# Kernel optimization log

Hardware: AMD Instinct MI355X
Metric: run time of the kernel (lower is better)

## Reference

```python
import jax, jax.numpy as jnp
import numpy as np

N_NODES = 50000
N_EDGES = 800000
H = 128
FF = 4 * H
SCALE = 30.0
EPS = 1e-5


def _layer_norm(x, g, b):
    mu = jnp.mean(x, axis=-1, keepdims=True)
    var = jnp.mean((x - mu) ** 2, axis=-1, keepdims=True)
    return (x - mu) * jax.lax.rsqrt(var + EPS) * g + b


def _linear(x, W, b):
    return x @ W.T + b


def setup_inputs() -> dict:
    key = jax.random.key(0)
    ks = jax.random.split(key, 16)
    s = lambda fan_in: 1.0 / np.sqrt(fan_in)
    inp = {
        "h_V": jax.random.normal(ks[0], (N_NODES, H), jnp.float32),
        "h_E": jax.random.normal(ks[1], (N_EDGES, H), jnp.float32),
        "src_idx": jax.random.randint(ks[2], (N_EDGES,), 0, N_NODES),
        "batch_id": jnp.zeros((N_NODES,), jnp.int32),
        "dst_idx": jax.random.randint(ks[3], (N_EDGES,), 0, N_NODES),
        "W1": jax.random.uniform(ks[4], (H, 3 * H), jnp.float32, -s(3 * H), s(3 * H)),
        "b1": jnp.zeros((H,), jnp.float32),
        "W2": jax.random.uniform(ks[5], (H, H), jnp.float32, -s(H), s(H)),
        "b2": jnp.zeros((H,), jnp.float32),
        "W3": jax.random.uniform(ks[6], (H, H), jnp.float32, -s(H), s(H)),
        "b3": jnp.zeros((H,), jnp.float32),
        "ln1_g": jnp.ones((H,), jnp.float32),
        "ln1_b": jnp.zeros((H,), jnp.float32),
        "ln2_g": jnp.ones((H,), jnp.float32),
        "ln2_b": jnp.zeros((H,), jnp.float32),
        "W_in": jax.random.uniform(ks[7], (FF, H), jnp.float32, -s(H), s(H)),
        "b_in": jnp.zeros((FF,), jnp.float32),
        "W_out": jax.random.uniform(ks[8], (H, FF), jnp.float32, -s(FF), s(FF)),
        "b_out": jnp.zeros((H,), jnp.float32),
    }
    return inp


def reference(h_V, h_E, src_idx, batch_id, dst_idx,
              W1, b1, W2, b2, W3, b3,
              ln1_g, ln1_b, ln2_g, ln2_b,
              W_in, b_in, W_out, b_out):
    # gather + concat: [E, 3H]
    h_EV = jnp.concatenate([h_V[src_idx], h_E, h_V[dst_idx]], axis=-1)
    # 3-layer edge MLP (exact GELU, matching torch default)
    h = jax.nn.gelu(_linear(h_EV, W1, b1), approximate=False)
    h = jax.nn.gelu(_linear(h, W2, b2), approximate=False)
    h_message = _linear(h, W3, b3)
    # scatter_mean by src_idx over N_NODES segments
    seg_sum = jax.ops.segment_sum(h_message, src_idx, num_segments=N_NODES)
    cnt = jax.ops.segment_sum(jnp.ones((h_message.shape[0],), h_message.dtype),
                              src_idx, num_segments=N_NODES)
    dh = seg_sum / jnp.maximum(cnt, 1.0)[:, None] / SCALE
    # residual + norm (dropout = identity in eval)
    h_V = _layer_norm(h_V + dh, ln1_g, ln1_b)
    # FFN
    dh = _linear(jax.nn.gelu(_linear(h_V, W_in, b_in), approximate=False), W_out, b_out)
    h_V = _layer_norm(h_V + dh, ln2_g, ln2_b)
    return h_V
```

## Files before the change

### kernel.cpp

```cpp
#include <hip/hip_runtime.h>

#define NE 800000
#define NN 50000
#define HD 128
#define FFD 512

typedef __bf16 bf16;
typedef bf16 bf16x8 __attribute__((ext_vector_type(8)));
typedef float f32x4 __attribute__((ext_vector_type(4)));

__device__ __forceinline__ float gelu_f(float x) {
    return 0.5f * x * (1.0f + erff(x * 0.70710678118654752f));
}

__device__ __forceinline__ bf16x8 cvt8(f32x4 a, f32x4 b) {
    bf16x8 t;
    t[0] = (bf16)a[0]; t[1] = (bf16)a[1]; t[2] = (bf16)a[2]; t[3] = (bf16)a[3];
    t[4] = (bf16)b[0]; t[5] = (bf16)b[1]; t[6] = (bf16)b[2]; t[7] = (bf16)b[3];
    return t;
}

__global__ void cvt_weights(const float* __restrict__ W1, const float* __restrict__ W2,
                            const float* __restrict__ W3, const float* __restrict__ Win,
                            const float* __restrict__ Wout, bf16* __restrict__ o) {
    int i = blockIdx.x * 256 + threadIdx.x;
    if (i < 49152)        o[i] = (bf16)W1[i];
    else if (i < 65536)   o[i] = (bf16)W2[i - 49152];
    else if (i < 81920)   o[i] = (bf16)W3[i - 65536];
    else if (i < 147456)  o[i] = (bf16)Win[i - 81920];
    else if (i < 212992)  o[i] = (bf16)Wout[i - 147456];
}

__global__ void hist_kernel(const int* __restrict__ src, int* __restrict__ cnt) {
    int i = blockIdx.x * 256 + threadIdx.x;
    if (i < NE) atomicAdd(cnt + src[i], 1);
}

__global__ __launch_bounds__(1024) void scan_kernel(const int* __restrict__ cnt,
                                                    int* __restrict__ head) {
    __shared__ int wsum[16];
    __shared__ int carry;
    const int tid = threadIdx.x, lane = tid & 63, w = tid >> 6;
    if (tid == 0) carry = 0;
    __syncthreads();
    for (int base = 0; base < NN; base += 1024) {
        int i = base + tid;
        int v = (i < NN) ? cnt[i] : 0;
        int x = v;
#pragma unroll
        for (int m = 1; m < 64; m <<= 1) {
            int y = __shfl_up(x, m, 64);
            if (lane >= m) x += y;
        }
        if (lane == 63) wsum[w] = x;
        __syncthreads();
        if (w == 0) {
            int s = (lane < 16) ? wsum[lane] : 0;
#pragma unroll
            for (int m = 1; m < 16; m <<= 1) {
                int y = __shfl_up(s, m, 64);
                if (lane >= m) s += y;
            }
            if (lane < 16) wsum[lane] = s;
        }
        __syncthreads();
        int excl = carry + (w > 0 ? wsum[w - 1] : 0) + x - v;
        if (i < NN) head[i] = excl;
        int total = wsum[15];
        __syncthreads();
        if (tid == 0) carry += total;
        __syncthreads();
    }
}

__global__ void scatter_perm(const int* __restrict__ src, int* __restrict__ head,
                             int* __restrict__ perm) {
    int i = blockIdx.x * 256 + threadIdx.x;
    if (i < NE) {
        int pos = atomicAdd(head + src[i], 1);
        perm[pos] = i;
    }
}

__global__ __launch_bounds__(256, 2) void edge_mlp(
    const float* __restrict__ hV, const float* __restrict__ hE,
    const int* __restrict__ src, const int* __restrict__ dst,
    const int* __restrict__ perm,
    const bf16* __restrict__ W1b, const bf16* __restrict__ W2b, const bf16* __restrict__ W3b,
    const float* __restrict__ b1, const float* __restrict__ b2, const float* __restrict__ b3,
    float* __restrict__ segsum)
{
    __shared__ __align__(16) char smem[128 * 132 * 4];
    bf16  (*lx)[136] = (bf16 (*)[136])smem;
    float (*lz)[132] = (float (*)[132])smem;
    __shared__ int ssrc[128];

    const int tid  = threadIdx.x;
    const int wave = tid >> 6, lane = tid & 63;
    const int wr = wave >> 1, wc = wave & 1;
    const int quad = lane >> 4, l16 = lane & 15;
    const int row0 = blockIdx.x * 128;

    if (tid < 128) ssrc[tid] = src[perm[row0 + tid]];

    int arow[4], asrc[4], adst[4];
#pragma unroll
    for (int rt = 0; rt < 4; ++rt) {
        int e = perm[row0 + wr * 64 + rt * 16 + l16];
        arow[rt] = e; asrc[rt] = src[e]; adst[rt] = dst[e];
    }

    f32x4 acc[4][4];
#pragma unroll
    for (int i = 0; i < 4; ++i)
#pragma unroll
        for (int j = 0; j < 4; ++j) acc[i][j] = (f32x4){0.f, 0.f, 0.f, 0.f};

#pragma unroll
    for (int ks = 0; ks < 12; ++ks) {
        const int k = ks * 32 + quad * 8;
        bf16x8 a[4];
#pragma unroll
        for (int rt = 0; rt < 4; ++rt) {
            const float* p;
            if (ks < 4)      p = hV + (size_t)asrc[rt] * HD + k;
            else if (ks < 8) p = hE + (size_t)arow[rt] * HD + (k - 128);
            else             p = hV + (size_t)adst[rt] * HD + (k - 256);
            f32x4 f0 = *(const f32x4*)p;
            f32x4 f1 = *(const f32x4*)(p + 4);
            a[rt] = cvt8(f0, f1);
        }
        bf16x8 b[4];
#pragma unroll
        for (int ct = 0; ct < 4; ++ct) {
            int col = wc * 64 + ct * 16 + l16;
            b[ct] = *(const bf16x8*)(W1b + (size_t)col * 384 + ks * 32 + quad * 8);
        }
#pragma unroll
        for (int rt = 0; rt < 4; ++rt)
#pragma unroll
            for (int ct = 0; ct < 4; ++ct)
                acc[rt][ct] = __builtin_amdgcn_mfma_f32_16x16x32_bf16(a[rt], b[ct], acc[rt][ct], 0, 0, 0);
    }

#pragma unroll
    for (int ct = 0; ct < 4; ++ct) {
        int col = wc * 64 + ct * 16 + l16;
        float bias = b1[col];
#pragma unroll
        for (int rt = 0; rt < 4; ++rt)
#pragma unroll
            for (int r = 0; r < 4; ++r)
                lx[wr * 64 + rt * 16 + quad * 4 + r][col] = (bf16)gelu_f(acc[rt][ct][r] + bias);
    }
    __syncthreads();

#pragma unroll
    for (int i = 0; i < 4; ++i)
#pragma unroll
        for (int j = 0; j < 4; ++j) acc[i][j] = (f32x4){0.f, 0.f, 0.f, 0.f};
#pragma unroll
    for (int ks = 0; ks < 4; ++ks) {
        bf16x8 a[4], b[4];
#pragma unroll
        for (int rt = 0; rt < 4; ++rt)
            a[rt] = *(const bf16x8*)&lx[wr * 64 + rt * 16 + l16][ks * 32 + quad * 8];
#pragma unroll
        for (int ct = 0; ct < 4; ++ct)
            b[ct] = *(const bf16x8*)(W2b + (size_t)(wc * 64 + ct * 16 + l16) * HD + ks * 32 + quad * 8);
#pragma unroll
        for (int rt = 0; rt < 4; ++rt)
#pragma unroll
            for (int ct = 0; ct < 4; ++ct)
                acc[rt][ct] = __builtin_amdgcn_mfma_f32_16x16x32_bf16(a[rt], b[ct], acc[rt][ct], 0, 0, 0);
    }
    __syncthreads();

#pragma unroll
    for (int ct = 0; ct < 4; ++ct) {
        int col = wc * 64 + ct * 16 + l16;
        float bias = b2[col];
#pragma unroll
        for (int rt = 0; rt < 4; ++rt)
#pragma unroll
            for (int r = 0; r < 4; ++r)
                lx[wr * 64 + rt * 16 + quad * 4 + r][col] = (bf16)gelu_f(acc[rt][ct][r] + bias);
    }
    __syncthreads();

#pragma unroll
    for (int i = 0; i < 4; ++i)
#pragma unroll
        for (int j = 0; j < 4; ++j) acc[i][j] = (f32x4){0.f, 0.f, 0.f, 0.f};
#pragma unroll
    for (int ks = 0; ks < 4; ++ks) {
        bf16x8 a[4], b[4];
#pragma unroll
        for (int rt = 0; rt < 4; ++rt)
            a[rt] = *(const bf16x8*)&lx[wr * 64 + rt * 16 + l16][ks * 32 + quad * 8];
#pragma unroll
        for (int ct = 0; ct < 4; ++ct)
            b[ct] = *(const bf16x8*)(W3b + (size_t)(wc * 64 + ct * 16 + l16) * HD + ks * 32 + quad * 8);
#pragma unroll
        for (int rt = 0; rt < 4; ++rt)
#pragma unroll
            for (int ct = 0; ct < 4; ++ct)
                acc[rt][ct] = __builtin_amdgcn_mfma_f32_16x16x32_bf16(a[rt], b[ct], acc[rt][ct], 0, 0, 0);
    }
    __syncthreads();

    float b3c[4];
#pragma unroll
    for (int ct = 0; ct < 4; ++ct) b3c[ct] = b3[wc * 64 + ct * 16 + l16];
#pragma unroll
    for (int ct = 0; ct < 4; ++ct)
#pragma unroll
        for (int rt = 0; rt < 4; ++rt)
#pragma unroll
            for (int r = 0; r < 4; ++r)
                lz[wr * 64 + rt * 16 + quad * 4 + r][wc * 64 + ct * 16 + l16] =
                    acc[rt][ct][r] + b3c[ct];
    __syncthreads();

    {
        const int c = tid & 127, h = tid >> 7;
        const int rbeg = h * 64, rend = rbeg + 64;
        float sum = lz[rbeg][c];
        int cur = ssrc[rbeg];
        for (int r = rbeg + 1; r < rend; ++r) {
            int s = ssrc[r];
            float v = lz[r][c];
            if (s != cur) {
                atomicAdd(segsum + (size_t)cur * HD + c, sum);
                cur = s; sum = v;
            } else {
                sum += v;
            }
        }
        atomicAdd(segsum + (size_t)cur * HD + c, sum);
    }
}

__global__ __launch_bounds__(256, 2) void node_ffn(
    const float* __restrict__ hV, float* __restrict__ out ,
    const int* __restrict__ cnt,
    const bf16* __restrict__ Winb, const bf16* __restrict__ Woutb,
    const float* __restrict__ bin, const float* __restrict__ bout,
    const float* __restrict__ g1, const float* __restrict__ be1,
    const float* __restrict__ g2, const float* __restrict__ be2)
{
    __shared__ bf16 lx[128][136];
    __shared__ bf16 ly[128][72];
    __shared__ float ps[128][2], pq[128][2];
    const int tid  = threadIdx.x;
    const int wave = tid >> 6, lane = tid & 63;
    const int wr = wave >> 1, wc = wave & 1;
    const int quad = lane >> 4, l16 = lane & 15;
    const int base = blockIdx.x * 128;

    for (int r = 0; r < 32; ++r) {
        int rl = wave * 32 + r;
        int node = base + rl;
        float u0 = 0.f, u1 = 0.f;
        bool valid = node < NN;
        if (valid) {
            int c = cnt[node];
            float inv = 1.0f / (30.0f * (float)(c > 1 ? c : 1));
            const float2 h = *(const float2*)(hV  + (size_t)node * HD + 2 * lane);
            const float2 s = *(const float2*)(out + (size_t)node * HD + 2 * lane);
            u0 = h.x + s.x * inv;
            u1 = h.y + s.y * inv;
        }
        float sm = u0 + u1, sq = u0 * u0 + u1 * u1;
#pragma unroll
        for (int m = 1; m < 64; m <<= 1) {
            sm += __shfl_xor(sm, m, 64);
            sq += __shfl_xor(sq, m, 64);
        }
        float mean = sm * (1.0f / 128.0f);
        float var  = sq * (1.0f / 128.0f) - mean * mean;
        float rstd = rsqrtf(var + 1e-5f);
        int c0 = 2 * lane;
        float x0 = valid ? ((u0 - mean) * rstd * g1[c0]     + be1[c0])     : 0.f;
        float x1 = valid ? ((u1 - mean) * rstd * g1[c0 + 1] + be1[c0 + 1]) : 0.f;
        lx[rl][c0] = (bf16)x0; lx[rl][c0 + 1] = (bf16)x1;
    }
    __syncthreads();

    f32x4 oacc[4][4];
#pragma unroll
    for (int i = 0; i < 4; ++i)
#pragma unroll
        for (int j = 0; j < 4; ++j) oacc[i][j] = (f32x4){0.f, 0.f, 0.f, 0.f};

    for (int c = 0; c < 8; ++c) {
        f32x4 a1[4][2];
#pragma unroll
        for (int i = 0; i < 4; ++i)
#pragma unroll
            for (int j = 0; j < 2; ++j) a1[i][j] = (f32x4){0.f, 0.f, 0.f, 0.f};
#pragma unroll
        for (int ks = 0; ks < 4; ++ks) {
            bf16x8 a[4], b[2];
#pragma unroll
            for (int rt = 0; rt < 4; ++rt)
                a[rt] = *(const bf16x8*)&lx[wr * 64 + rt * 16 + l16][ks * 32 + quad * 8];
#pragma unroll
            for (int ct = 0; ct < 2; ++ct) {
                int f = c * 64 + wc * 32 + ct * 16 + l16;
                b[ct] = *(const bf16x8*)(Winb + (size_t)f * HD + ks * 32 + quad * 8);
            }
#pragma unroll
            for (int rt = 0; rt < 4; ++rt)
#pragma unroll
                for (int ct = 0; ct < 2; ++ct)
                    a1[rt][ct] = __builtin_amdgcn_mfma_f32_16x16x32_bf16(a[rt], b[ct], a1[rt][ct], 0, 0, 0);
        }
        __syncthreads();
#pragma unroll
        for (int ct = 0; ct < 2; ++ct) {
            int f  = c * 64 + wc * 32 + ct * 16 + l16;
            int fl = wc * 32 + ct * 16 + l16;
            float bias = bin[f];
#pragma unroll
            for (int rt = 0; rt < 4; ++rt)
#pragma unroll
                for (int r = 0; r < 4; ++r)
                    ly[wr * 64 + rt * 16 + quad * 4 + r][fl] = (bf16)gelu_f(a1[rt][ct][r] + bias);
        }
        __syncthreads();
#pragma unroll
        for (int ks = 0; ks < 2; ++ks) {
            bf16x8 a[4], b[4];
#pragma unroll
            for (int rt = 0; rt < 4; ++rt)
                a[rt] = *(const bf16x8*)&ly[wr * 64 + rt * 16 + l16][ks * 32 + quad * 8];
#pragma unroll
            for (int ct = 0; ct < 4; ++ct) {
                int o = wc * 64 + ct * 16 + l16;
                b[ct] = *(const bf16x8*)(Woutb + (size_t)o * FFD + c * 64 + ks * 32 + quad * 8);
            }
#pragma unroll
            for (int rt = 0; rt < 4; ++rt)
#pragma unroll
                for (int ct = 0; ct < 4; ++ct)
                    oacc[rt][ct] = __builtin_amdgcn_mfma_f32_16x16x32_bf16(a[rt], b[ct], oacc[rt][ct], 0, 0, 0);
        }
    }

    float bo[4];
#pragma unroll
    for (int ct = 0; ct < 4; ++ct) bo[ct] = bout[wc * 64 + ct * 16 + l16];
#pragma unroll
    for (int rt = 0; rt < 4; ++rt)
#pragma unroll
        for (int r = 0; r < 4; ++r) {
            int rl = wr * 64 + rt * 16 + quad * 4 + r;
            float sm = 0.f, sq = 0.f;
#pragma unroll
            for (int ct = 0; ct < 4; ++ct) {
                int o = wc * 64 + ct * 16 + l16;
                float zz = oacc[rt][ct][r] + bo[ct] + (float)lx[rl][o];
                oacc[rt][ct][r] = zz;
                sm += zz; sq += zz * zz;
            }
#pragma unroll
            for (int m = 1; m < 16; m <<= 1) {
                sm += __shfl_xor(sm, m, 64);
                sq += __shfl_xor(sq, m, 64);
            }
            if (l16 == 0) { ps[rl][wc] = sm; pq[rl][wc] = sq; }
        }
    __syncthreads();
#pragma unroll
    for (int rt = 0; rt < 4; ++rt)
#pragma unroll
        for (int r = 0; r < 4; ++r) {
            int rl = wr * 64 + rt * 16 + quad * 4 + r;
            int node = base + rl;
            float S = ps[rl][0] + ps[rl][1];
            float Q = pq[rl][0] + pq[rl][1];
            float mean = S * (1.0f / 128.0f);
            float var  = Q * (1.0f / 128.0f) - mean * mean;
            float rstd = rsqrtf(var + 1e-5f);
            if (node < NN) {
#pragma unroll
                for (int ct = 0; ct < 4; ++ct) {
                    int o = wc * 64 + ct * 16 + l16;
                    out[(size_t)node * HD + o] = (oacc[rt][ct][r] - mean) * rstd * g2[o] + be2[o];
                }
            }
        }
}

extern "C" void kernel_launch(void* const* d_in, const int* in_sizes, int n_in,
                              void* d_out, int out_size, void* d_ws, size_t ws_size,
                              hipStream_t stream) {
    const float* hV   = (const float*)d_in[0];
    const float* hE   = (const float*)d_in[1];
    const int*   src  = (const int*)d_in[2];
    const int*   dst  = (const int*)d_in[4];
    const float* W1   = (const float*)d_in[5];
    const float* b1   = (const float*)d_in[6];
    const float* W2   = (const float*)d_in[7];
    const float* b2   = (const float*)d_in[8];
    const float* W3   = (const float*)d_in[9];
    const float* b3   = (const float*)d_in[10];
    const float* g1   = (const float*)d_in[11];
    const float* be1  = (const float*)d_in[12];
    const float* g2   = (const float*)d_in[13];
    const float* be2  = (const float*)d_in[14];
    const float* Win  = (const float*)d_in[15];
    const float* bin  = (const float*)d_in[16];
    const float* Wout = (const float*)d_in[17];
    const float* bout = (const float*)d_in[18];

    float* out = (float*)d_out;
    bf16* wbf  = (bf16*)d_ws;
    int*  cnt  = (int*)((char*)d_ws + 425984);
    int*  head = (int*)((char*)d_ws + 625984);
    int*  perm = (int*)((char*)d_ws + 825984);

    hipMemsetAsync(d_out, 0, (size_t)NN * HD * sizeof(float), stream);
    hipMemsetAsync(cnt, 0, NN * sizeof(int), stream);

    cvt_weights<<<832, 256, 0, stream>>>(W1, W2, W3, Win, Wout, wbf);
    hist_kernel<<<(NE + 255) / 256, 256, 0, stream>>>(src, cnt);
    scan_kernel<<<1, 1024, 0, stream>>>(cnt, head);
    scatter_perm<<<(NE + 255) / 256, 256, 0, stream>>>(src, head, perm);
    edge_mlp<<<NE / 128, 256, 0, stream>>>(hV, hE, src, dst, perm,
                                           wbf, wbf + 49152, wbf + 65536,
                                           b1, b2, b3, out);
    node_ffn<<<(NN + 127) / 128, 256, 0, stream>>>(hV, out, cnt,
                                                   wbf + 81920, wbf + 147456,
                                                   bin, bout, g1, be1, g2, be2);
}
```

Before: 1.385 ms.

## Parallelize scan, double-buffer edge gather through LDS, shrink LDS, vectorize LayerNorm

Replaces the single-block serial prefix scan with a three-kernel multi-block scan. In edge_mlp, each thread now loads one row-slice of the gathered input once and stages it as bf16 in a double-buffered LDS tile, prefetching the next k-slice while MFMAs run. This replaces the redundant per-wave global gathers. The output staging buffer is halved and reduced in two column passes, which cuts LDS so three blocks per CU fit (launch bounds raised to 3). Node LayerNorm now uses four threads per row with vectorized loads instead of one wave per row with shuffles. The cost is extra barriers per k-step and possible register pressure at the higher occupancy target.

```diff
diff --git a/kernel.cpp b/kernel.cpp
--- a/kernel.cpp
+++ b/kernel.cpp
@@ -36,41 +36,54 @@
     if (i < NE) atomicAdd(cnt + src[i], 1);
 }
 
-__global__ __launch_bounds__(1024) void scan_kernel(const int* __restrict__ cnt,
-                                                    int* __restrict__ head) {
-    __shared__ int wsum[16];
-    __shared__ int carry;
-    const int tid = threadIdx.x, lane = tid & 63, w = tid >> 6;
-    if (tid == 0) carry = 0;
-    __syncthreads();
-    for (int base = 0; base < NN; base += 1024) {
-        int i = base + tid;
-        int v = (i < NN) ? cnt[i] : 0;
-        int x = v;
-#pragma unroll
-        for (int m = 1; m < 64; m <<= 1) {
-            int y = __shfl_up(x, m, 64);
-            if (lane >= m) x += y;
-        }
-        if (lane == 63) wsum[w] = x;
-        __syncthreads();
-        if (w == 0) {
-            int s = (lane < 16) ? wsum[lane] : 0;
-#pragma unroll
-            for (int m = 1; m < 16; m <<= 1) {
-                int y = __shfl_up(s, m, 64);
-                if (lane >= m) s += y;
-            }
-            if (lane < 16) wsum[lane] = s;
-        }
-        __syncthreads();
-        int excl = carry + (w > 0 ? wsum[w - 1] : 0) + x - v;
-        if (i < NN) head[i] = excl;
-        int total = wsum[15];
-        __syncthreads();
-        if (tid == 0) carry += total;
-        __syncthreads();
-    }
+__global__ void scan_a(const int* __restrict__ cnt, int* __restrict__ head,
+                       int* __restrict__ bsum) {
+    __shared__ int ws[4];
+    const int t = threadIdx.x, lane = t & 63, w = t >> 6;
+    int i = blockIdx.x * 256 + t;
+    int v = (i < NN) ? cnt[i] : 0;
+    int x = v;
+#pragma unroll
+    for (int m = 1; m < 64; m <<= 1) {
+        int y = __shfl_up(x, m, 64);
+        if (lane >= m) x += y;
+    }
+    if (lane == 63) ws[w] = x;
+    __syncthreads();
+    if (t == 0) {
+        int s = 0;
+#pragma unroll
+        for (int j = 0; j < 4; ++j) { int tv = ws[j]; ws[j] = s; s += tv; }
+        bsum[blockIdx.x] = s;
+    }
+    __syncthreads();
+    if (i < NN) head[i] = ws[w] + x - v;
+}
+
+__global__ void scan_b(int* __restrict__ bsum, int nb) {
+    __shared__ int ws[4];
+    const int t = threadIdx.x, lane = t & 63, w = t >> 6;
+    int v = (t < nb) ? bsum[t] : 0;
+    int x = v;
+#pragma unroll
+    for (int m = 1; m < 64; m <<= 1) {
+        int y = __shfl_up(x, m, 64);
+        if (lane >= m) x += y;
+    }
+    if (lane == 63) ws[w] = x;
+    __syncthreads();
+    if (t == 0) {
+        int s = 0;
+#pragma unroll
+        for (int j = 0; j < 4; ++j) { int tv = ws[j]; ws[j] = s; s += tv; }
+    }
+    __syncthreads();
+    if (t < nb) bsum[t] = ws[w] + x - v;
+}
+
+__global__ void scan_c(int* __restrict__ head, const int* __restrict__ bsum) {
+    int i = blockIdx.x * 256 + threadIdx.x;
+    if (i < NN) head[i] += bsum[blockIdx.x];
 }
 
 __global__ void scatter_perm(const int* __restrict__ src, int* __restrict__ head,
@@ -82,7 +95,7 @@
     }
 }
 
-__global__ __launch_bounds__(256, 2) void edge_mlp(
+__global__ __launch_bounds__(256, 3) void edge_mlp(
     const float* __restrict__ hV, const float* __restrict__ hE,
     const int* __restrict__ src, const int* __restrict__ dst,
     const int* __restrict__ perm,
@@ -90,10 +103,11 @@
     const float* __restrict__ b1, const float* __restrict__ b2, const float* __restrict__ b3,
     float* __restrict__ segsum)
 {
-    __shared__ __align__(16) char smem[128 * 132 * 4];
+    __shared__ bf16 As[2][128][36];
+    __shared__ __align__(16) char smem[128 * 136 * 2];
+    __shared__ int ssrc[128];
     bf16  (*lx)[136] = (bf16 (*)[136])smem;
-    float (*lz)[132] = (float (*)[132])smem;
-    __shared__ int ssrc[128];
+    float (*lz)[68]  = (float (*)[68])smem;
 
     const int tid  = threadIdx.x;
     const int wave = tid >> 6, lane = tid & 63;
@@ -101,14 +115,19 @@
     const int quad = lane >> 4, l16 = lane & 15;
     const int row0 = blockIdx.x * 128;
 
-    if (tid < 128) ssrc[tid] = src[perm[row0 + tid]];
-
-    int arow[4], asrc[4], adst[4];
-#pragma unroll
-    for (int rt = 0; rt < 4; ++rt) {
-        int e = perm[row0 + wr * 64 + rt * 16 + l16];
-        arow[rt] = e; asrc[rt] = src[e]; adst[rt] = dst[e];
-    }
+    const int myrow = tid >> 1, khalf = (tid & 1) * 16;
+    const int me    = perm[row0 + myrow];
+    const int mysrc = src[me], mydst = dst[me];
+    if ((tid & 1) == 0) ssrc[myrow] = mysrc;
+
+    {
+        const float* p = hV + (size_t)mysrc * HD + khalf;
+        f32x4 s0 = *(const f32x4*)p,       s1 = *(const f32x4*)(p + 4);
+        f32x4 s2 = *(const f32x4*)(p + 8), s3 = *(const f32x4*)(p + 12);
+        *(bf16x8*)&As[0][myrow][khalf]     = cvt8(s0, s1);
+        *(bf16x8*)&As[0][myrow][khalf + 8] = cvt8(s2, s3);
+    }
+    __syncthreads();
 
     f32x4 acc[4][4];
 #pragma unroll
@@ -116,21 +135,23 @@
 #pragma unroll
         for (int j = 0; j < 4; ++j) acc[i][j] = (f32x4){0.f, 0.f, 0.f, 0.f};
 
-#pragma unroll
     for (int ks = 0; ks < 12; ++ks) {
-        const int k = ks * 32 + quad * 8;
-        bf16x8 a[4];
-#pragma unroll
-        for (int rt = 0; rt < 4; ++rt) {
+        const int cur = ks & 1, nxt = cur ^ 1;
+        const bool more = ks < 11;
+        f32x4 s0, s1, s2, s3;
+        if (more) {
+            const int kn = (ks + 1) * 32 + khalf;
             const float* p;
-            if (ks < 4)      p = hV + (size_t)asrc[rt] * HD + k;
-            else if (ks < 8) p = hE + (size_t)arow[rt] * HD + (k - 128);
-            else             p = hV + (size_t)adst[rt] * HD + (k - 256);
-            f32x4 f0 = *(const f32x4*)p;
-            f32x4 f1 = *(const f32x4*)(p + 4);
-            a[rt] = cvt8(f0, f1);
-        }
-        bf16x8 b[4];
+            if (kn < 128)      p = hV + (size_t)mysrc * HD + kn;
+            else if (kn < 256) p = hE + (size_t)me    * HD + (kn - 128);
+            else               p = hV + (size_t)mydst * HD + (kn - 256);
+            s0 = *(const f32x4*)p;       s1 = *(const f32x4*)(p + 4);
+            s2 = *(const f32x4*)(p + 8); s3 = *(const f32x4*)(p + 12);
+        }
+        bf16x8 a[4], b[4];
+#pragma unroll
+        for (int rt = 0; rt < 4; ++rt)
+            a[rt] = *(const bf16x8*)&As[cur][wr * 64 + rt * 16 + l16][quad * 8];
 #pragma unroll
         for (int ct = 0; ct < 4; ++ct) {
             int col = wc * 64 + ct * 16 + l16;
@@ -141,6 +162,11 @@
 #pragma unroll
             for (int ct = 0; ct < 4; ++ct)
                 acc[rt][ct] = __builtin_amdgcn_mfma_f32_16x16x32_bf16(a[rt], b[ct], acc[rt][ct], 0, 0, 0);
+        if (more) {
+            *(bf16x8*)&As[nxt][myrow][khalf]     = cvt8(s0, s1);
+            *(bf16x8*)&As[nxt][myrow][khalf + 8] = cvt8(s2, s3);
+        }
+        __syncthreads();
     }
 
 #pragma unroll
@@ -207,37 +233,40 @@
             for (int ct = 0; ct < 4; ++ct)
                 acc[rt][ct] = __builtin_amdgcn_mfma_f32_16x16x32_bf16(a[rt], b[ct], acc[rt][ct], 0, 0, 0);
     }
-    __syncthreads();
 
     float b3c[4];
 #pragma unroll
     for (int ct = 0; ct < 4; ++ct) b3c[ct] = b3[wc * 64 + ct * 16 + l16];
-#pragma unroll
-    for (int ct = 0; ct < 4; ++ct)
-#pragma unroll
-        for (int rt = 0; rt < 4; ++rt)
-#pragma unroll
-            for (int r = 0; r < 4; ++r)
-                lz[wr * 64 + rt * 16 + quad * 4 + r][wc * 64 + ct * 16 + l16] =
-                    acc[rt][ct][r] + b3c[ct];
-    __syncthreads();
-
-    {
-        const int c = tid & 127, h = tid >> 7;
-        const int rbeg = h * 64, rend = rbeg + 64;
+
+#pragma unroll
+    for (int half = 0; half < 2; ++half) {
+        __syncthreads();
+        if (wc == half) {
+#pragma unroll
+            for (int ct = 0; ct < 4; ++ct)
+#pragma unroll
+                for (int rt = 0; rt < 4; ++rt)
+#pragma unroll
+                    for (int r = 0; r < 4; ++r)
+                        lz[wr * 64 + rt * 16 + quad * 4 + r][ct * 16 + l16] =
+                            acc[rt][ct][r] + b3c[ct];
+        }
+        __syncthreads();
+        const int c = tid & 63, h = tid >> 6;
+        const int rbeg = h * 32, rend = rbeg + 32;
         float sum = lz[rbeg][c];
         int cur = ssrc[rbeg];
         for (int r = rbeg + 1; r < rend; ++r) {
             int s = ssrc[r];
             float v = lz[r][c];
             if (s != cur) {
-                atomicAdd(segsum + (size_t)cur * HD + c, sum);
+                atomicAdd(segsum + (size_t)cur * HD + half * 64 + c, sum);
                 cur = s; sum = v;
             } else {
                 sum += v;
             }
         }
-        atomicAdd(segsum + (size_t)cur * HD + c, sum);
+        atomicAdd(segsum + (size_t)cur * HD + half * 64 + c, sum);
     }
 }
 
@@ -258,32 +287,49 @@
     const int quad = lane >> 4, l16 = lane & 15;
     const int base = blockIdx.x * 128;
 
-    for (int r = 0; r < 32; ++r) {
-        int rl = wave * 32 + r;
-        int node = base + rl;
-        float u0 = 0.f, u1 = 0.f;
-        bool valid = node < NN;
+#pragma unroll
+    for (int p = 0; p < 2; ++p) {
+        const int rl = p * 64 + (tid >> 2);
+        const int qf = tid & 3;
+        const int node = base + rl;
+        const bool valid = node < NN;
+        float u[32];
+        float sm = 0.f, sq = 0.f;
         if (valid) {
             int c = cnt[node];
             float inv = 1.0f / (30.0f * (float)(c > 1 ? c : 1));
-            const float2 h = *(const float2*)(hV  + (size_t)node * HD + 2 * lane);
-            const float2 s = *(const float2*)(out + (size_t)node * HD + 2 * lane);
-            u0 = h.x + s.x * inv;
-            u1 = h.y + s.y * inv;
-        }
-        float sm = u0 + u1, sq = u0 * u0 + u1 * u1;
-#pragma unroll
-        for (int m = 1; m < 64; m <<= 1) {
-            sm += __shfl_xor(sm, m, 64);
-            sq += __shfl_xor(sq, m, 64);
-        }
+            const float* ph = hV  + (size_t)node * HD + qf * 32;
+            const float* pz = out + (size_t)node * HD + qf * 32;
+#pragma unroll
+            for (int i = 0; i < 8; ++i) {
+                f32x4 a = *(const f32x4*)(ph + 4 * i);
+                f32x4 s = *(const f32x4*)(pz + 4 * i);
+#pragma unroll
+                for (int j = 0; j < 4; ++j) {
+                    float uu = a[j] + s[j] * inv;
+                    u[4 * i + j] = uu; sm += uu; sq += uu * uu;
+                }
+            }
+        } else {
+#pragma unroll
+            for (int i = 0; i < 32; ++i) u[i] = 0.f;
+        }
+        sm += __shfl_xor(sm, 1, 64); sq += __shfl_xor(sq, 1, 64);
+        sm += __shfl_xor(sm, 2, 64); sq += __shfl_xor(sq, 2, 64);
         float mean = sm * (1.0f / 128.0f);
         float var  = sq * (1.0f / 128.0f) - mean * mean;
         float rstd = rsqrtf(var + 1e-5f);
-        int c0 = 2 * lane;
-        float x0 = valid ? ((u0 - mean) * rstd * g1[c0]     + be1[c0])     : 0.f;
-        float x1 = valid ? ((u1 - mean) * rstd * g1[c0 + 1] + be1[c0 + 1]) : 0.f;
-        lx[rl][c0] = (bf16)x0; lx[rl][c0 + 1] = (bf16)x1;
+#pragma unroll
+        for (int i = 0; i < 4; ++i) {
+            bf16x8 w;
+#pragma unroll
+            for (int j = 0; j < 8; ++j) {
+                int col = qf * 32 + i * 8 + j;
+                float x = valid ? ((u[i * 8 + j] - mean) * rstd * g1[col] + be1[col]) : 0.f;
+                w[j] = (bf16)x;
+            }
+            *(bf16x8*)&lx[rl][qf * 32 + i * 8] = w;
+        }
     }
     __syncthreads();
 
@@ -420,13 +466,18 @@
     int*  cnt  = (int*)((char*)d_ws + 425984);
     int*  head = (int*)((char*)d_ws + 625984);
     int*  perm = (int*)((char*)d_ws + 825984);
+    int*  bsum = (int*)((char*)d_ws + 4025984);
+
+    const int NB = (NN + 255) / 256;
 
     hipMemsetAsync(d_out, 0, (size_t)NN * HD * sizeof(float), stream);
     hipMemsetAsync(cnt, 0, NN * sizeof(int), stream);
 
     cvt_weights<<<832, 256, 0, stream>>>(W1, W2, W3, Win, Wout, wbf);
     hist_kernel<<<(NE + 255) / 256, 256, 0, stream>>>(src, cnt);
-    scan_kernel<<<1, 1024, 0, stream>>>(cnt, head);
+    scan_a<<<NB, 256, 0, stream>>>(cnt, head, bsum);
+    scan_b<<<1, 256, 0, stream>>>(bsum, NB);
+    scan_c<<<NB, 256, 0, stream>>>(head, bsum);
     scatter_perm<<<(NE + 255) / 256, 256, 0, stream>>>(src, head, perm);
     edge_mlp<<<NE / 128, 256, 0, stream>>>(hV, hE, src, dst, perm,
                                            wbf, wbf + 49152, wbf + 65536,
```

Result: faster. 1.119 ms (-19.2%).
